# Optimization experiments

Hardware: AMD Instinct MI355X
Metric: run time of the kernel (lower is better)

The kernel has to match this reference:

```python
import jax, jax.numpy as jnp
import numpy as np

B, F = 16384, 2048


def setup_inputs() -> dict:
    key = jax.random.key(0)
    k0, k1 = jax.random.split(key)
    x0 = jax.random.normal(k0, (B, F), dtype=jnp.float32)
    x = jax.random.normal(k1, (B, F), dtype=jnp.float32)
    # Parameters as initialized by the torch module
    weights = jnp.ones((F,), dtype=jnp.float32)
    bias = jnp.zeros((F,), dtype=jnp.float32)
    return {"x0": x0, "x": x, "weights": weights, "bias": bias}


def reference(x0, x, weights, bias):
    # torch: bmm(x0[:, :, None], x[:, None, :]) @ weights + bias + x
    # The [B,F,F] outer product contracted with weights over the last axis
    # equals x0 * (x . weights), computed in O(B*F) without the F^2 tensor.
    xw = jnp.einsum('bf,f->b', x, weights)  # [B]
    return x0 * xw[:, None] + bias + x
```

## Files before the change

### kernel.cpp

```cpp
#include <hip/hip_runtime.h>


#define F_DIM 2048
#define SLOTS 8

__global__ __launch_bounds__(256) void cross_row_kernel(
    const float* __restrict__ x0,
    const float* __restrict__ x,
    const float* __restrict__ w,
    const float* __restrict__ bias,
    float* __restrict__ out)
{
    const int wave = threadIdx.x >> 6;
    const int lane = threadIdx.x & 63;
    const long long b = (long long)blockIdx.x * 4 + wave;
    const long long row = b * (long long)F_DIM;

    const float4* __restrict__ x4  = (const float4*)(x  + row);
    const float4* __restrict__ x04 = (const float4*)(x0 + row);
    const float4* __restrict__ w4  = (const float4*)w;
    const float4* __restrict__ bi4 = (const float4*)bias;
    float4*       __restrict__ o4  = (float4*)(out + row);

    float4 xr[SLOTS], x0r[SLOTS];
    #pragma unroll
    for (int i = 0; i < SLOTS; ++i) xr[i]  = x4 [lane + 64 * i];
    #pragma unroll
    for (int i = 0; i < SLOTS; ++i) x0r[i] = x04[lane + 64 * i];

    float partial = 0.0f;
    #pragma unroll
    for (int i = 0; i < SLOTS; ++i) {
        const float4 wv = w4[lane + 64 * i];
        partial += xr[i].x * wv.x + xr[i].y * wv.y
                 + xr[i].z * wv.z + xr[i].w * wv.w;
    }

    #pragma unroll
    for (int off = 32; off > 0; off >>= 1)
        partial += __shfl_xor(partial, off, 64);
    const float dot = partial;

    #pragma unroll
    for (int i = 0; i < SLOTS; ++i) {
        const float4 bv = bi4[lane + 64 * i];
        float4 o;
        o.x = x0r[i].x * dot + (bv.x + xr[i].x);
        o.y = x0r[i].y * dot + (bv.y + xr[i].y);
        o.z = x0r[i].z * dot + (bv.z + xr[i].z);
        o.w = x0r[i].w * dot + (bv.w + xr[i].w);
        o4[lane + 64 * i] = o;
    }
}

extern "C" void kernel_launch(void* const* d_in, const int* in_sizes, int n_in,
                              void* d_out, int out_size, void* d_ws, size_t ws_size,
                              hipStream_t stream) {
    const float* x0   = (const float*)d_in[0];
    const float* x    = (const float*)d_in[1];
    const float* w    = (const float*)d_in[2];
    const float* bias = (const float*)d_in[3];
    float* out = (float*)d_out;

    const int B = in_sizes[0] / F_DIM;
    cross_row_kernel<<<B / 4, 256, 0, stream>>>(x0, x, w, bias, out);
}
```

Baseline: 311.3 us.

## Process four rows per wave with register double-buffering and nontemporal memory ops

Each wave now handles four consecutive rows. Weights and bias are loaded into registers once per wave, and the next row's x and x0 are prefetched into a second register buffer while the current row is reduced and written. x0 loads and output stores use nontemporal hints to avoid polluting the cache. This cuts redundant weight and bias loads and gives more memory-level parallelism per wave. In exchange it roughly doubles register use and launches four times fewer blocks, which may lower occupancy.

Result: no change. 307.7 us (-1.2%).

```diff
diff --git a/kernel.cpp b/kernel.cpp
--- a/kernel.cpp
+++ b/kernel.cpp
@@ -3,6 +3,9 @@
 
 #define F_DIM 2048
 #define SLOTS 8
+#define ROWS  4
+
+typedef float f4 __attribute__((ext_vector_type(4)));
 
 __global__ __launch_bounds__(256) void cross_row_kernel(
     const float* __restrict__ x0,
@@ -13,43 +16,67 @@
 {
     const int wave = threadIdx.x >> 6;
     const int lane = threadIdx.x & 63;
-    const long long b = (long long)blockIdx.x * 4 + wave;
-    const long long row = b * (long long)F_DIM;
+    const long long wid  = (long long)blockIdx.x * 4 + wave;
+    const long long row0 = wid * ROWS;
 
-    const float4* __restrict__ x4  = (const float4*)(x  + row);
-    const float4* __restrict__ x04 = (const float4*)(x0 + row);
-    const float4* __restrict__ w4  = (const float4*)w;
-    const float4* __restrict__ bi4 = (const float4*)bias;
-    float4*       __restrict__ o4  = (float4*)(out + row);
+    const f4* __restrict__ w4  = (const f4*)w;
+    const f4* __restrict__ bi4 = (const f4*)bias;
 
-    float4 xr[SLOTS], x0r[SLOTS];
+    f4 wr[SLOTS], br[SLOTS];
     #pragma unroll
-    for (int i = 0; i < SLOTS; ++i) xr[i]  = x4 [lane + 64 * i];
+    for (int i = 0; i < SLOTS; ++i) wr[i] = w4 [lane + 64 * i];
     #pragma unroll
-    for (int i = 0; i < SLOTS; ++i) x0r[i] = x04[lane + 64 * i];
+    for (int i = 0; i < SLOTS; ++i) br[i] = bi4[lane + 64 * i];
 
-    float partial = 0.0f;
-    #pragma unroll
-    for (int i = 0; i < SLOTS; ++i) {
-        const float4 wv = w4[lane + 64 * i];
-        partial += xr[i].x * wv.x + xr[i].y * wv.y
-                 + xr[i].z * wv.z + xr[i].w * wv.w;
-    }
+    const f4* __restrict__ xbase  = (const f4*)(x  + row0 * F_DIM);
+    const f4* __restrict__ x0base = (const f4*)(x0 + row0 * F_DIM);
+    f4*       __restrict__ obase  = (f4*)(out + row0 * F_DIM);
+    const int F4 = F_DIM / 4;
+
+    f4 xa[SLOTS], x0a[SLOTS];
+    f4 xb[SLOTS], x0b[SLOTS];
 
     #pragma unroll
-    for (int off = 32; off > 0; off >>= 1)
-        partial += __shfl_xor(partial, off, 64);
-    const float dot = partial;
+    for (int i = 0; i < SLOTS; ++i) xa[i] = xbase[lane + 64 * i];
+    #pragma unroll
+    for (int i = 0; i < SLOTS; ++i)
+        x0a[i] = __builtin_nontemporal_load(&x0base[lane + 64 * i]);
 
     #pragma unroll
-    for (int i = 0; i < SLOTS; ++i) {
-        const float4 bv = bi4[lane + 64 * i];
-        float4 o;
-        o.x = x0r[i].x * dot + (bv.x + xr[i].x);
-        o.y = x0r[i].y * dot + (bv.y + xr[i].y);
-        o.z = x0r[i].z * dot + (bv.z + xr[i].z);
-        o.w = x0r[i].w * dot + (bv.w + xr[i].w);
-        o4[lane + 64 * i] = o;
+    for (int r = 0; r < ROWS; ++r) {
+        if (r + 1 < ROWS) {
+            const f4* __restrict__ xn  = xbase  + (r + 1) * F4;
+            const f4* __restrict__ x0n = x0base + (r + 1) * F4;
+            #pragma unroll
+            for (int i = 0; i < SLOTS; ++i) xb[i] = xn[lane + 64 * i];
+            #pragma unroll
+            for (int i = 0; i < SLOTS; ++i)
+                x0b[i] = __builtin_nontemporal_load(&x0n[lane + 64 * i]);
+        }
+
+        float partial = 0.0f;
+        #pragma unroll
+        for (int i = 0; i < SLOTS; ++i)
+            partial += xa[i][0] * wr[i][0] + xa[i][1] * wr[i][1]
+                     + xa[i][2] * wr[i][2] + xa[i][3] * wr[i][3];
+        #pragma unroll
+        for (int off = 32; off > 0; off >>= 1)
+            partial += __shfl_xor(partial, off, 64);
+        const float dot = partial;
+
+        f4* __restrict__ o = obase + r * F4;
+        #pragma unroll
+        for (int i = 0; i < SLOTS; ++i) {
+            f4 ov;
+            ov[0] = x0a[i][0] * dot + (br[i][0] + xa[i][0]);
+            ov[1] = x0a[i][1] * dot + (br[i][1] + xa[i][1]);
+            ov[2] = x0a[i][2] * dot + (br[i][2] + xa[i][2]);
+            ov[3] = x0a[i][3] * dot + (br[i][3] + xa[i][3]);
+            __builtin_nontemporal_store(ov, &o[lane + 64 * i]);
+        }
+
+        #pragma unroll
+        for (int i = 0; i < SLOTS; ++i) { xa[i] = xb[i]; x0a[i] = x0b[i]; }
     }
 }
 
@@ -63,5 +90,6 @@
     float* out = (float*)d_out;
 
     const int B = in_sizes[0] / F_DIM;
-    cross_row_kernel<<<B / 4, 256, 0, stream>>>(x0, x, w, bias, out);
+    const int blocks = B / (4 * ROWS);
+    cross_row_kernel<<<blocks, 256, 0, stream>>>(x0, x, w, bias, out);
 }
```

## Split row-dot and elementwise epilogue into two grid-stride kernels

Applied to the files above, without the earlier changes.

Separates the per-row dot product into its own persistent kernel, which keeps the weights in registers and double-buffers the next row's x loads. It writes the dots to workspace, and a second flat grid-stride kernel then computes the elementwise output. The aim is to raise memory-level parallelism and bandwidth use over the one-wave-per-row design. The cost is an extra full read of x and a second kernel launch.

Measured after the change: 321.3 us. 1.03x slower.

```diff
diff --git a/kernel.cpp b/kernel.cpp
--- a/kernel.cpp
+++ b/kernel.cpp
@@ -2,54 +2,95 @@
 
 
 #define F_DIM 2048
+#define F4_ROW 512
 #define SLOTS 8
 
-__global__ __launch_bounds__(256) void cross_row_kernel(
-    const float* __restrict__ x0,
+typedef float f4 __attribute__((ext_vector_type(4)));
+
+__global__ __launch_bounds__(256) void dot_kernel(
     const float* __restrict__ x,
     const float* __restrict__ w,
-    const float* __restrict__ bias,
-    float* __restrict__ out)
+    float* __restrict__ dots,
+    int B)
 {
     const int wave = threadIdx.x >> 6;
     const int lane = threadIdx.x & 63;
-    const long long b = (long long)blockIdx.x * 4 + wave;
-    const long long row = b * (long long)F_DIM;
+    const int wid  = blockIdx.x * 4 + wave;
+    const int nw   = gridDim.x * 4;
 
-    const float4* __restrict__ x4  = (const float4*)(x  + row);
-    const float4* __restrict__ x04 = (const float4*)(x0 + row);
-    const float4* __restrict__ w4  = (const float4*)w;
-    const float4* __restrict__ bi4 = (const float4*)bias;
-    float4*       __restrict__ o4  = (float4*)(out + row);
+    const f4* __restrict__ w4 = (const f4*)w;
+    f4 wr[SLOTS];
+    #pragma unroll
+    for (int i = 0; i < SLOTS; ++i) wr[i] = w4[lane + 64 * i];
 
-    float4 xr[SLOTS], x0r[SLOTS];
-    #pragma unroll
-    for (int i = 0; i < SLOTS; ++i) xr[i]  = x4 [lane + 64 * i];
-    #pragma unroll
-    for (int i = 0; i < SLOTS; ++i) x0r[i] = x04[lane + 64 * i];
+    f4 xa[SLOTS], xb[SLOTS];
+    int row = wid;
+    if (row < B) {
+        const f4* __restrict__ xr = (const f4*)(x + (long long)row * F_DIM);
+        #pragma unroll
+        for (int i = 0; i < SLOTS; ++i) xa[i] = xr[lane + 64 * i];
+    }
+    for (; row < B; row += nw) {
+        const int nrow = row + nw;
+        if (nrow < B) {
+            const f4* __restrict__ xn = (const f4*)(x + (long long)nrow * F_DIM);
+            #pragma unroll
+            for (int i = 0; i < SLOTS; ++i) xb[i] = xn[lane + 64 * i];
+        }
+        float p = 0.0f;
+        #pragma unroll
+        for (int i = 0; i < SLOTS; ++i)
+            p += xa[i][0] * wr[i][0] + xa[i][1] * wr[i][1]
+               + xa[i][2] * wr[i][2] + xa[i][3] * wr[i][3];
+        #pragma unroll
+        for (int off = 32; off > 0; off >>= 1)
+            p += __shfl_xor(p, off, 64);
+        if (lane == 0) dots[row] = p;
+        #pragma unroll
+        for (int i = 0; i < SLOTS; ++i) xa[i] = xb[i];
+    }
+}
 
-    float partial = 0.0f;
-    #pragma unroll
-    for (int i = 0; i < SLOTS; ++i) {
-        const float4 wv = w4[lane + 64 * i];
-        partial += xr[i].x * wv.x + xr[i].y * wv.y
-                 + xr[i].z * wv.z + xr[i].w * wv.w;
-    }
+__global__ __launch_bounds__(256) void epi_kernel(
+    const float* __restrict__ x0,
+    const float* __restrict__ x,
+    const float* __restrict__ bias,
+    const float* __restrict__ dots,
+    float* __restrict__ out,
+    long long total_f4)
+{
+    const f4* __restrict__ x04 = (const f4*)x0;
+    const f4* __restrict__ x4  = (const f4*)x;
+    const f4* __restrict__ bi4 = (const f4*)bias;
+    f4*       __restrict__ o4  = (f4*)out;
 
-    #pragma unroll
-    for (int off = 32; off > 0; off >>= 1)
-        partial += __shfl_xor(partial, off, 64);
-    const float dot = partial;
-
-    #pragma unroll
-    for (int i = 0; i < SLOTS; ++i) {
-        const float4 bv = bi4[lane + 64 * i];
-        float4 o;
-        o.x = x0r[i].x * dot + (bv.x + xr[i].x);
-        o.y = x0r[i].y * dot + (bv.y + xr[i].y);
-        o.z = x0r[i].z * dot + (bv.z + xr[i].z);
-        o.w = x0r[i].w * dot + (bv.w + xr[i].w);
-        o4[lane + 64 * i] = o;
+    const long long stride = (long long)gridDim.x * 1024;
+    for (long long gb = (long long)blockIdx.x * 1024; gb < total_f4; gb += stride) {
+        const long long g0 = gb + threadIdx.x;
+        if (gb + 1024 <= total_f4) {
+            f4 a0 = x04[g0], a1 = x04[g0 + 256], a2 = x04[g0 + 512], a3 = x04[g0 + 768];
+            f4 b0 = x4 [g0], b1 = x4 [g0 + 256], b2 = x4 [g0 + 512], b3 = x4 [g0 + 768];
+            float d0 = dots[(g0)       >> 9];
+            float d1 = dots[(g0 + 256) >> 9];
+            float d2 = dots[(g0 + 512) >> 9];
+            float d3 = dots[(g0 + 768) >> 9];
+            f4 v0 = bi4[(g0)       & 511];
+            f4 v1 = bi4[(g0 + 256) & 511];
+            f4 v2 = bi4[(g0 + 512) & 511];
+            f4 v3 = bi4[(g0 + 768) & 511];
+            o4[g0]       = a0 * d0 + (v0 + b0);
+            o4[g0 + 256] = a1 * d1 + (v1 + b1);
+            o4[g0 + 512] = a2 * d2 + (v2 + b2);
+            o4[g0 + 768] = a3 * d3 + (v3 + b3);
+        } else {
+            for (int k = 0; k < 4; ++k) {
+                const long long g = g0 + k * 256;
+                if (g < total_f4) {
+                    f4 a = x04[g], b = x4[g];
+                    o4[g] = a * dots[g >> 9] + (bi4[g & 511] + b);
+                }
+            }
+        }
     }
 }
 
@@ -60,8 +101,12 @@
     const float* x    = (const float*)d_in[1];
     const float* w    = (const float*)d_in[2];
     const float* bias = (const float*)d_in[3];
-    float* out = (float*)d_out;
+    float* out  = (float*)d_out;
+    float* dots = (float*)d_ws;
 
     const int B = in_sizes[0] / F_DIM;
-    cross_row_kernel<<<B / 4, 256, 0, stream>>>(x0, x, w, bias, out);
+    const long long total_f4 = (long long)B * F4_ROW;
+
+    dot_kernel<<<1024, 256, 0, stream>>>(x, w, dots, B);
+    epi_kernel<<<2048, 256, 0, stream>>>(x0, x, bias, dots, out, total_f4);
 }
```
